# Performance work log

Hardware: AMD Instinct MI355X
Metric: run time of the kernel (lower is better)

The kernel has to match this reference:

```python
import jax, jax.numpy as jnp
import numpy as np

H = 8  # number_heads

def setup_inputs() -> dict:
    key = jax.random.key(0)
    ks = jax.random.split(key, 10)
    B, Nx, Ny, Qd, Kd, Vd = 4, 2048, 2048, 512, 512, 512
    s = 0.02
    return {
        "X": jax.random.normal(ks[0], (B, Nx, Qd), jnp.float32),
        "Y": jax.random.normal(ks[1], (B, Ny, Kd), jnp.float32),
        "Wq": jax.random.normal(ks[2], (Vd, Qd), jnp.float32) * s,
        "bq": jax.random.normal(ks[3], (Vd,), jnp.float32) * s,
        "Wk": jax.random.normal(ks[4], (Vd, Kd), jnp.float32) * s,
        "bk": jax.random.normal(ks[5], (Vd,), jnp.float32) * s,
        "Wv": jax.random.normal(ks[6], (Vd, Kd), jnp.float32) * s,
        "bv": jax.random.normal(ks[7], (Vd,), jnp.float32) * s,
        "Wo": jax.random.normal(ks[8], (Vd, Vd), jnp.float32) * s,
        "bo": jax.random.normal(ks[9], (Vd,), jnp.float32) * s,
    }

def reference(X, Y, Wq, bq, Wk, bk, Wv, bv, Wo, bo):
    B, Nq, _ = X.shape
    Nk = Y.shape[1]
    Vd = Wq.shape[0]
    d = Vd // H  # head dim (dim_split)
    # QKV projections (torch Linear: x @ W^T + b)
    Q = (X @ Wq.T + bq).reshape(B, Nq, H, d)
    K = (Y @ Wk.T + bk).reshape(B, Nk, H, d)
    V = (Y @ Wv.T + bv).reshape(B, Nk, H, d)
    # attention: softmax(Q K^T / sqrt(d)) per head
    scores = jnp.einsum("bqhd,bkhd->bhqk", Q, K) / jnp.sqrt(jnp.float32(d))
    attn = jax.nn.softmax(scores, axis=-1)
    # residual on Q (pre-output-proj), per the original: O = Q_split + Attn @ V_split
    O = Q + jnp.einsum("bhqk,bkhd->bqhd", attn, V)
    O = O.reshape(B, Nq, Vd)  # concat heads back
    return O @ Wo.T + bo
```

## Files before the change

### kernel.cpp

```cpp
#include <hip/hip_runtime.h>
#include <hip/hip_bf16.h>

typedef unsigned short u16;
typedef __attribute__((ext_vector_type(4))) float f32x4;
typedef __attribute__((ext_vector_type(16))) float f32x16;
typedef __attribute__((ext_vector_type(8))) short bf16x8;
typedef __attribute__((ext_vector_type(4))) int i32x4;
typedef __attribute__((ext_vector_type(4))) unsigned short u16x4;

#define DEVI static __device__ __forceinline__

DEVI u16 f2bf(float f) {
  __hip_bfloat16 h = __float2bfloat16(f);
  return *reinterpret_cast<u16*>(&h);
}
DEVI float bf2f(u16 u) {
  unsigned int x = ((unsigned int)u) << 16;
  return __uint_as_float(x);
}
DEVI float exp2a(float x) {
  float r;
  asm("v_exp_f32 %0, %1" : "=v"(r) : "v"(x));
  return r;
}
DEVI int cvtpk(float lo, float hi) {
  int r;
  asm("v_cvt_pk_bf16_f32 %0, %1, %2" : "=v"(r) : "v"(lo), "v"(hi));
  return r;
}
DEVI f32x16 mfma32(bf16x8 a, bf16x8 b, f32x16 c) {
  return __builtin_amdgcn_mfma_f32_32x32x16_bf16(a, b, c, 0, 0, 0);
}
DEVI float xhalf_sum(float x) {
  float a = x, b;
  asm volatile("v_mov_b32 %0, %1" : "=v"(b) : "v"(x));
  asm volatile("v_permlane32_swap_b32 %0, %1" : "+v"(a), "+v"(b));
  return a + b;
}

DEVI void gload_lds16(const void* g, void* l) {
  __builtin_amdgcn_global_load_lds(
      (const __attribute__((address_space(1))) unsigned int*)g,
      (__attribute__((address_space(3))) unsigned int*)l, 16, 0, 0);
}

#define BAR() __builtin_amdgcn_s_barrier()
#define WAITV0() asm volatile("s_waitcnt vmcnt(0)" ::: "memory")
#define WAITV4() asm volatile("s_waitcnt vmcnt(4)" ::: "memory")

__global__ __launch_bounds__(256) void k_convall(
    const float* __restrict__ X, const float* __restrict__ Y,
    const float* __restrict__ Wq, const float* __restrict__ Wk,
    const float* __restrict__ Wv, const float* __restrict__ Wo,
    u16* __restrict__ Xb, u16* __restrict__ Yb, u16* __restrict__ Wb) {
  long i = ((long)blockIdx.x * 256 + threadIdx.x) * 8;
  const float* s;
  u16* d;
  long off;
  if (i < 4194304) {
    s = X; d = Xb; off = i;
  } else if (i < 8388608) {
    s = Y; d = Yb; off = i - 4194304;
  } else {
    long w = (i - 8388608) >> 18;
    off = (i - 8388608) & 262143;
    s = w == 0 ? Wq : w == 1 ? Wk : w == 2 ? Wv : Wo;
    d = Wb + w * 262144;
  }
  f32x4 a = *(const f32x4*)(s + off);
  f32x4 b = *(const f32x4*)(s + off + 4);
  bf16x8 v;
#pragma unroll
  for (int j = 0; j < 4; ++j) {
    v[j]     = (short)f2bf(a[j]);
    v[4 + j] = (short)f2bf(b[j]);
  }
  *(bf16x8*)(d + off) = v;
}

struct GemmAcc { f32x4 acc[4][2]; };

DEVI void gemm_body(const u16* __restrict__ A, const u16* __restrict__ Bw,
                    int m0, int n0, char* sm, GemmAcc& G) {
  const int tid = threadIdx.x;
  const int wid = tid >> 6, lane = tid & 63;
  const int g = lane >> 4, li = lane & 15;
  const int wr = wid >> 1, wc = wid & 1;

  int arow[4], acol[4];
#pragma unroll
  for (int i = 0; i < 4; ++i) {
    int P0 = ((i * 4 + wid) << 10) + lane * 16;
    int L0 = P0 ^ (((P0 >> 7) & 7) << 4);
    arow[i] = L0 >> 7;
    acol[i] = L0 & 127;
  }

#pragma unroll
  for (int mr = 0; mr < 4; ++mr)
#pragma unroll
    for (int nr = 0; nr < 2; ++nr) G.acc[mr][nr] = (f32x4){0.f, 0.f, 0.f, 0.f};

  auto stage = [&](int kt, int half) {
    char* As = sm + half * 24576;
    char* Bs = As + 16384;
    const int k0b = kt * 128;
#pragma unroll
    for (int i = 0; i < 4; ++i)
      gload_lds16((const char*)A + (size_t)(m0 + arow[i]) * 1024 + k0b + acol[i],
                  As + ((i * 4 + wid) << 10));
#pragma unroll
    for (int i = 0; i < 2; ++i)
      gload_lds16((const char*)Bw + (size_t)(n0 + arow[i]) * 1024 + k0b + acol[i],
                  Bs + ((i * 4 + wid) << 10));
  };

  stage(0, 0);
#pragma unroll 1
  for (int kt = 0; kt < 8; ++kt) {
    const int half = kt & 1;
    if (kt < 7) {
      stage(kt + 1, half ^ 1);
      asm volatile("s_waitcnt vmcnt(6)" ::: "memory");
    } else {
      asm volatile("s_waitcnt vmcnt(0)" ::: "memory");
    }
    BAR();
    const char* As = sm + half * 24576;
    const char* Bs = As + 16384;
#pragma unroll
    for (int ks = 0; ks < 2; ++ks) {
      bf16x8 af[4], bfr[2];
#pragma unroll
      for (int mr = 0; mr < 4; ++mr) {
        int row = wr * 64 + mr * 16 + li;
        int L = row * 128 + ks * 64 + g * 16;
        int P = L ^ ((row & 7) << 4);
        af[mr] = *(const bf16x8*)(As + P);
      }
#pragma unroll
      for (int nr = 0; nr < 2; ++nr) {
        int row = wc * 32 + nr * 16 + li;
        int L = row * 128 + ks * 64 + g * 16;
        int P = L ^ ((row & 7) << 4);
        bfr[nr] = *(const bf16x8*)(Bs + P);
      }
#pragma unroll
      for (int mr = 0; mr < 4; ++mr)
#pragma unroll
        for (int nr = 0; nr < 2; ++nr)
          G.acc[mr][nr] = __builtin_amdgcn_mfma_f32_16x16x32_bf16(
              af[mr], bfr[nr], G.acc[mr][nr], 0, 0, 0);
    }
    BAR();
  }
}

__global__ __launch_bounds__(256) void k_gemm_qkv(
    const u16* __restrict__ Xb, const u16* __restrict__ Yb,
    const u16* __restrict__ Wall, const float* __restrict__ bq,
    const float* __restrict__ bk, const float* __restrict__ bv,
    u16* __restrict__ Qb, u16* __restrict__ Kb, u16* __restrict__ Vtb) {
  __shared__ __align__(16) char sm[49152];
  const int z = blockIdx.z;
  int lin = blockIdx.x + 8 * blockIdx.y;
  int xcd = lin & 7, slot = lin >> 3;

  const u16 *Ag, *Bg;
  int m0, n0;
  if (z == 2) {
    Ag = Wall + 2 * 262144;
    Bg = Yb;
    m0 = (slot >> 4) * 128;
    n0 = (xcd * 16 + (slot & 15)) * 64;
  } else {
    Ag = z ? Yb : Xb;
    Bg = Wall + (size_t)z * 262144;
    m0 = (xcd * 8 + (slot >> 3)) * 128;
    n0 = (slot & 7) * 64;
  }

  GemmAcc G;
  gemm_body(Ag, Bg, m0, n0, sm, G);

  const int tid = threadIdx.x;
  const int wid = tid >> 6, lane = tid & 63;
  const int g = lane >> 4, li = lane & 15;
  const int wr = wid >> 1, wc = wid & 1;

  if (z <= 1) {
    u16* Cout = z ? Kb : Qb;
    const float* bias = z ? bk : bq;
#pragma unroll
    for (int nr = 0; nr < 2; ++nr) {
      int col = n0 + wc * 32 + nr * 16 + li;
      float bvv = bias[col];
#pragma unroll
      for (int mr = 0; mr < 4; ++mr) {
#pragma unroll
        for (int j = 0; j < 4; ++j) {
          int row = m0 + wr * 64 + mr * 16 + g * 4 + j;
          float v = G.acc[mr][nr][j] + bvv;
          int b = row >> 11, nn = row & 2047, h = col >> 6, dd = col & 63;
          Cout[(((size_t)(b * 8 + h) << 11) + nn) * 64 + dd] = f2bf(v);
        }
      }
    }
  } else {
#pragma unroll
    for (int mr = 0; mr < 4; ++mr) {
#pragma unroll
      for (int j = 0; j < 4; ++j) {
        int row = m0 + wr * 64 + mr * 16 + g * 4 + j;
        float bvv = bv[row];
        int hh = row >> 6, dd = row & 63;
#pragma unroll
        for (int nr = 0; nr < 2; ++nr) {
          int col = n0 + wc * 32 + nr * 16 + li;
          int b = col >> 11, nn = col & 2047;
          Vtb[(((size_t)(b * 8 + hh) * 64) + dd) * 2048 + nn] =
              f2bf(G.acc[mr][nr][j] + bvv);
        }
      }
    }
  }
}

__global__ __launch_bounds__(256) void k_gemm_out(const u16* __restrict__ A,
                                                  const u16* __restrict__ Bw,
                                                  const float* __restrict__ bias,
                                                  float* __restrict__ Cout) {
  __shared__ __align__(16) char sm[49152];
  int lin = blockIdx.x + 8 * blockIdx.y;
  int xcd = lin & 7, slot = lin >> 3;
  int by = xcd * 8 + (slot >> 3), bx = slot & 7;
  const int m0 = by * 128, n0 = bx * 64;

  GemmAcc G;
  gemm_body(A, Bw, m0, n0, sm, G);

  const int tid = threadIdx.x;
  const int wid = tid >> 6, lane = tid & 63;
  const int g = lane >> 4, li = lane & 15;
  const int wr = wid >> 1, wc = wid & 1;
#pragma unroll
  for (int nr = 0; nr < 2; ++nr) {
    int col = n0 + wc * 32 + nr * 16 + li;
    float bvv = bias[col];
#pragma unroll
    for (int mr = 0; mr < 4; ++mr) {
#pragma unroll
      for (int j = 0; j < 4; ++j) {
        int row = m0 + wr * 64 + mr * 16 + g * 4 + j;
        Cout[(size_t)row * 512 + col] = G.acc[mr][nr][j] + bvv;
      }
    }
  }
}

DEVI void attn_tile64(const char* L, int KB, const int* v4, const bf16x8* qf,
                      f32x16& o0, f32x16& o1, float& lsum) {
  const int VB = KB + 8192;
  const f32x16 Z = {};
  f32x16 s0, s1;
  bf16x8 kf;
  kf = *(const bf16x8*)(L + KB + v4[0]);        s0 = mfma32(kf, qf[0], Z);
  kf = *(const bf16x8*)(L + KB + 4096 + v4[0]); s1 = mfma32(kf, qf[0], Z);
  kf = *(const bf16x8*)(L + KB + v4[1]);        s0 = mfma32(kf, qf[1], s0);
  kf = *(const bf16x8*)(L + KB + 4096 + v4[1]); s1 = mfma32(kf, qf[1], s1);
  kf = *(const bf16x8*)(L + KB + v4[2]);        s0 = mfma32(kf, qf[2], s0);
  kf = *(const bf16x8*)(L + KB + 4096 + v4[2]); s1 = mfma32(kf, qf[2], s1);
  kf = *(const bf16x8*)(L + KB + v4[3]);        s0 = mfma32(kf, qf[3], s0);
  kf = *(const bf16x8*)(L + KB + 4096 + v4[3]); s1 = mfma32(kf, qf[3], s1);

#pragma unroll
  for (int i = 0; i < 16; ++i) s0[i] = exp2a(s0[i]);
#pragma unroll
  for (int i = 0; i < 16; ++i) s1[i] = exp2a(s1[i]);
  float t8[8];
#pragma unroll
  for (int i = 0; i < 8; ++i)
    t8[i] = (s0[2 * i] + s0[2 * i + 1]) + (s1[2 * i] + s1[2 * i + 1]);
  lsum += ((t8[0] + t8[1]) + (t8[2] + t8[3])) + ((t8[4] + t8[5]) + (t8[6] + t8[7]));

#pragma unroll
  for (int half = 0; half < 2; ++half) {
    const f32x16& sp = half ? s1 : s0;
#pragma unroll
    for (int kt = 0; kt < 2; ++kt) {
      const int base = kt * 8;
      int a0 = cvtpk(sp[base + 0], sp[base + 1]);
      int a1 = cvtpk(sp[base + 2], sp[base + 3]);
      int b0 = cvtpk(sp[base + 4], sp[base + 5]);
      int b1 = cvtpk(sp[base + 6], sp[base + 7]);
      asm volatile("v_permlane32_swap_b32 %0, %1" : "+v"(a0), "+v"(b0));
      asm volatile("v_permlane32_swap_b32 %0, %1" : "+v"(a1), "+v"(b1));
      i32x4 pi = {a0, a1, b0, b1};
      bf16x8 pb = __builtin_bit_cast(bf16x8, pi);
      const int s = half * 2 + kt;
      bf16x8 va = *(const bf16x8*)(L + VB + v4[s]);
      o0 = mfma32(va, pb, o0);
      va = *(const bf16x8*)(L + VB + 4096 + v4[s]);
      o1 = mfma32(va, pb, o1);
    }
  }
}

__global__ __launch_bounds__(512, 4) void k_attn(const u16* __restrict__ Qb,
                                                 const u16* __restrict__ Kb,
                                                 const u16* __restrict__ Vt,
                                                 u16* __restrict__ Ob) {
  __shared__ __align__(16) char lds[65536];
  const int tid = threadIdx.x, wid = tid >> 6, lane = tid & 63;
  const int li = lane & 31, h = lane >> 5;
  const int grp = wid >> 2, w4 = wid & 3;

  const int lin = blockIdx.x;
  const int xcd = lin & 7, slot = lin >> 3;
  const int bh = xcd * 4 + (slot >> 4);
  const int qt = slot & 15;
  const int start = (slot * 3) & 15;

  const u16* Qh = Qb + ((size_t)bh << 11) * 64;
  const u16* Kh = Kb + ((size_t)bh << 11) * 64;
  const u16* Vh = Vt + (size_t)bh * 64 * 2048;

  int v4[4];
  {
    const int swz = (li & 7) << 4;
#pragma unroll
    for (int s = 0; s < 4; ++s) v4[s] = li * 128 + ((s * 32 + h * 16) ^ swz);
  }

  const int q = qt * 128 + w4 * 32 + li;
  const float C2 = 0.18033688f;
  bf16x8 qf[4];
#pragma unroll
  for (int k4 = 0; k4 < 4; ++k4) {
    bf16x8 f = *(const bf16x8*)(Qh + (size_t)q * 64 + k4 * 16 + h * 8);
    bf16x8 r;
#pragma unroll
    for (int e = 0; e < 4; ++e) {
      int p = cvtpk(bf2f((u16)f[2 * e]) * C2, bf2f((u16)f[2 * e + 1]) * C2);
      r[2 * e]     = (short)(p & 0xffff);
      r[2 * e + 1] = (short)((unsigned)p >> 16);
    }
    qf[k4] = r;
  }

  char* gb = lds + grp * 32768;
  const char* Lg = gb;
  int ksrc[2], vsrc[2];
#pragma unroll
  for (int j = 0; j < 2; ++j) {
    int P0 = w4 * 2048 + j * 1024 + lane * 16;
    int L0 = P0 ^ (((P0 >> 7) & 7) << 4);
    ksrc[j] = L0;
    vsrc[j] = (L0 >> 7) * 4096 + (L0 & 127);
  }

  auto T = [&](int n) { return grp * 16 + ((start + n) & 15); };
  auto stage = [&](int tt, int bb) {
#pragma unroll
    for (int j = 0; j < 2; ++j)
      gload_lds16((const char*)Kh + (size_t)tt * 8192 + ksrc[j],
                  gb + bb + w4 * 2048 + j * 1024);
#pragma unroll
    for (int j = 0; j < 2; ++j)
      gload_lds16((const char*)Vh + (size_t)tt * 128 + vsrc[j],
                  gb + bb + 8192 + w4 * 2048 + j * 1024);
  };

  f32x16 o0 = {}, o1 = {};
  float lsum = 0.f;

  stage(T(0), 0);
  stage(T(1), 16384);
  WAITV4();
  BAR();

#pragma unroll 1
  for (int it = 0; it < 14; ++it) {
    const int cur = (it & 1) * 16384;
    attn_tile64(Lg, cur, v4, qf, o0, o1, lsum);
    BAR();
    stage(T(it + 2), cur);
    WAITV4();
    BAR();
  }
  attn_tile64(Lg, 0, v4, qf, o0, o1, lsum);
  WAITV0();
  BAR();
  attn_tile64(Lg, 16384, v4, qf, o0, o1, lsum);

  __syncthreads();
  if (grp == 1) {
#pragma unroll
    for (int j = 0; j < 8; ++j) {
      const f32x16& o = (j < 4) ? o0 : o1;
      const int s2 = (j & 3) * 4;
      f32x4 c = {o[s2 + 0], o[s2 + 1], o[s2 + 2], o[s2 + 3]};
      *(f32x4*)(lds + w4 * 8192 + j * 1024 + lane * 16) = c;
    }
    ((float*)(lds + 32768))[w4 * 64 + lane] = lsum;
  }
  __syncthreads();
  if (grp == 0) {
#pragma unroll
    for (int j = 0; j < 8; ++j) {
      f32x4 c = *(const f32x4*)(lds + w4 * 8192 + j * 1024 + lane * 16);
      f32x16& o = (j < 4) ? o0 : o1;
      const int s2 = (j & 3) * 4;
      o[s2 + 0] += c[0]; o[s2 + 1] += c[1]; o[s2 + 2] += c[2]; o[s2 + 3] += c[3];
    }
    lsum += ((const float*)(lds + 32768))[w4 * 64 + lane];
    const float inv = 1.0f / xhalf_sum(lsum);

    const int b = bh >> 3, head = bh & 7;
    u16* orow = Ob + ((size_t)(b * 2048 + q)) * 512 + head * 64;
    const u16* qrow = Qh + (size_t)q * 64;
#pragma unroll
    for (int dt = 0; dt < 2; ++dt) {
      const f32x16& o = dt ? o1 : o0;
#pragma unroll
      for (int s2 = 0; s2 < 4; ++s2) {
        int d0 = dt * 32 + s2 * 8 + h * 4;
        u16x4 qv = *(const u16x4*)(qrow + d0);
        u16x4 w;
#pragma unroll
        for (int j = 0; j < 4; ++j)
          w[j] = f2bf(fmaf(o[s2 * 4 + j], inv, bf2f(qv[j])));
        *(u16x4*)(orow + d0) = w;
      }
    }
  }
}

extern "C" void kernel_launch(void* const* d_in, const int* in_sizes, int n_in,
                              void* d_out, int out_size, void* d_ws, size_t ws_size,
                              hipStream_t stream) {
  const float* X  = (const float*)d_in[0];
  const float* Y  = (const float*)d_in[1];
  const float* Wq = (const float*)d_in[2];
  const float* bq = (const float*)d_in[3];
  const float* Wk = (const float*)d_in[4];
  const float* bk = (const float*)d_in[5];
  const float* Wv = (const float*)d_in[6];
  const float* bv = (const float*)d_in[7];
  const float* Wo = (const float*)d_in[8];
  const float* bo = (const float*)d_in[9];

  char* ws = (char*)d_ws;
  u16* Xb  = (u16*)(ws);
  u16* Yb  = (u16*)(ws + (size_t)(8  << 20));
  u16* Wb  = (u16*)(ws + (size_t)(16 << 20));
  u16* Qb  = (u16*)(ws + (size_t)(18 << 20));
  u16* Kb  = (u16*)(ws + (size_t)(26 << 20));
  u16* Vtb = (u16*)(ws + (size_t)(34 << 20));
  u16* Ob  = (u16*)(ws + (size_t)(42 << 20));

  k_convall<<<4608, 256, 0, stream>>>(X, Y, Wq, Wk, Wv, Wo, Xb, Yb, Wb);

  k_gemm_qkv<<<dim3(8, 64, 3), 256, 0, stream>>>(Xb, Yb, Wb, bq, bk, bv, Qb, Kb, Vtb);

  k_attn<<<512, 512, 0, stream>>>(Qb, Kb, Vtb, Ob);

  k_gemm_out<<<dim3(8, 64), 256, 0, stream>>>(Ob, Wb + 3 * 262144, bo, (float*)d_out);
}
```

Baseline: 86.80 us.

## Process two query tiles per wave in attention to reuse K/V fragments

```diff
diff --git a/kernel.cpp b/kernel.cpp
--- a/kernel.cpp
+++ b/kernel.cpp
@@ -258,67 +258,85 @@
   }
 }
 
-DEVI void attn_tile64(const char* L, int KB, const int* v4, const bf16x8* qf,
-                      f32x16& o0, f32x16& o1, float& lsum) {
-  const int VB = KB + 8192;
+DEVI void attn_phase(const char* L, int kb, int vb, const int* v4, int sv0, int sv1,
+                     const bf16x8* qfA, const bf16x8* qfB,
+                     f32x16& oA0, f32x16& oA1, f32x16& oB0, f32x16& oB1,
+                     float& lsumA, float& lsumB) {
   const f32x16 Z = {};
-  f32x16 s0, s1;
+  f32x16 sA, sB;
   bf16x8 kf;
-  kf = *(const bf16x8*)(L + KB + v4[0]);        s0 = mfma32(kf, qf[0], Z);
-  kf = *(const bf16x8*)(L + KB + 4096 + v4[0]); s1 = mfma32(kf, qf[0], Z);
-  kf = *(const bf16x8*)(L + KB + v4[1]);        s0 = mfma32(kf, qf[1], s0);
-  kf = *(const bf16x8*)(L + KB + 4096 + v4[1]); s1 = mfma32(kf, qf[1], s1);
-  kf = *(const bf16x8*)(L + KB + v4[2]);        s0 = mfma32(kf, qf[2], s0);
-  kf = *(const bf16x8*)(L + KB + 4096 + v4[2]); s1 = mfma32(kf, qf[2], s1);
-  kf = *(const bf16x8*)(L + KB + v4[3]);        s0 = mfma32(kf, qf[3], s0);
-  kf = *(const bf16x8*)(L + KB + 4096 + v4[3]); s1 = mfma32(kf, qf[3], s1);
-
-#pragma unroll
-  for (int i = 0; i < 16; ++i) s0[i] = exp2a(s0[i]);
-#pragma unroll
-  for (int i = 0; i < 16; ++i) s1[i] = exp2a(s1[i]);
-  float t8[8];
-#pragma unroll
-  for (int i = 0; i < 8; ++i)
-    t8[i] = (s0[2 * i] + s0[2 * i + 1]) + (s1[2 * i] + s1[2 * i + 1]);
-  lsum += ((t8[0] + t8[1]) + (t8[2] + t8[3])) + ((t8[4] + t8[5]) + (t8[6] + t8[7]));
-
-#pragma unroll
-  for (int half = 0; half < 2; ++half) {
-    const f32x16& sp = half ? s1 : s0;
-#pragma unroll
-    for (int kt = 0; kt < 2; ++kt) {
-      const int base = kt * 8;
-      int a0 = cvtpk(sp[base + 0], sp[base + 1]);
-      int a1 = cvtpk(sp[base + 2], sp[base + 3]);
-      int b0 = cvtpk(sp[base + 4], sp[base + 5]);
-      int b1 = cvtpk(sp[base + 6], sp[base + 7]);
-      asm volatile("v_permlane32_swap_b32 %0, %1" : "+v"(a0), "+v"(b0));
-      asm volatile("v_permlane32_swap_b32 %0, %1" : "+v"(a1), "+v"(b1));
-      i32x4 pi = {a0, a1, b0, b1};
-      bf16x8 pb = __builtin_bit_cast(bf16x8, pi);
-      const int s = half * 2 + kt;
-      bf16x8 va = *(const bf16x8*)(L + VB + v4[s]);
-      o0 = mfma32(va, pb, o0);
-      va = *(const bf16x8*)(L + VB + 4096 + v4[s]);
-      o1 = mfma32(va, pb, o1);
-    }
-  }
-}
-
-__global__ __launch_bounds__(512, 4) void k_attn(const u16* __restrict__ Qb,
+  kf = *(const bf16x8*)(L + kb + v4[0]);
+  sA = mfma32(kf, qfA[0], Z);  sB = mfma32(kf, qfB[0], Z);
+  kf = *(const bf16x8*)(L + kb + v4[1]);
+  sA = mfma32(kf, qfA[1], sA); sB = mfma32(kf, qfB[1], sB);
+  kf = *(const bf16x8*)(L + kb + v4[2]);
+  sA = mfma32(kf, qfA[2], sA); sB = mfma32(kf, qfB[2], sB);
+  kf = *(const bf16x8*)(L + kb + v4[3]);
+  sA = mfma32(kf, qfA[3], sA); sB = mfma32(kf, qfB[3], sB);
+
+  bf16x8 va0l = *(const bf16x8*)(L + vb + v4[sv0]);
+  bf16x8 va0h = *(const bf16x8*)(L + vb + 4096 + v4[sv0]);
+  bf16x8 va1l = *(const bf16x8*)(L + vb + v4[sv1]);
+  bf16x8 va1h = *(const bf16x8*)(L + vb + 4096 + v4[sv1]);
+
+#pragma unroll
+  for (int i = 0; i < 16; ++i) sA[i] = exp2a(sA[i]);
+#pragma unroll
+  for (int i = 0; i < 16; ++i) sB[i] = exp2a(sB[i]);
+  float tA[4], tB[4];
+#pragma unroll
+  for (int i = 0; i < 4; ++i) {
+    tA[i] = (sA[4 * i] + sA[4 * i + 1]) + (sA[4 * i + 2] + sA[4 * i + 3]);
+    tB[i] = (sB[4 * i] + sB[4 * i + 1]) + (sB[4 * i + 2] + sB[4 * i + 3]);
+  }
+  lsumA += (tA[0] + tA[1]) + (tA[2] + tA[3]);
+  lsumB += (tB[0] + tB[1]) + (tB[2] + tB[3]);
+
+  bf16x8 pbA[2], pbB[2];
+#pragma unroll
+  for (int kt = 0; kt < 2; ++kt) {
+    const int base = kt * 8;
+    int a0 = cvtpk(sA[base + 0], sA[base + 1]);
+    int a1 = cvtpk(sA[base + 2], sA[base + 3]);
+    int b0 = cvtpk(sA[base + 4], sA[base + 5]);
+    int b1 = cvtpk(sA[base + 6], sA[base + 7]);
+    asm volatile("v_permlane32_swap_b32 %0, %1" : "+v"(a0), "+v"(b0));
+    asm volatile("v_permlane32_swap_b32 %0, %1" : "+v"(a1), "+v"(b1));
+    i32x4 pi = {a0, a1, b0, b1};
+    pbA[kt] = __builtin_bit_cast(bf16x8, pi);
+    int c0 = cvtpk(sB[base + 0], sB[base + 1]);
+    int c1 = cvtpk(sB[base + 2], sB[base + 3]);
+    int d0 = cvtpk(sB[base + 4], sB[base + 5]);
+    int d1 = cvtpk(sB[base + 6], sB[base + 7]);
+    asm volatile("v_permlane32_swap_b32 %0, %1" : "+v"(c0), "+v"(d0));
+    asm volatile("v_permlane32_swap_b32 %0, %1" : "+v"(c1), "+v"(d1));
+    i32x4 qi = {c0, c1, d0, d1};
+    pbB[kt] = __builtin_bit_cast(bf16x8, qi);
+  }
+
+  oA0 = mfma32(va0l, pbA[0], oA0);
+  oB0 = mfma32(va0l, pbB[0], oB0);
+  oA1 = mfma32(va0h, pbA[0], oA1);
+  oB1 = mfma32(va0h, pbB[0], oB1);
+  oA0 = mfma32(va1l, pbA[1], oA0);
+  oB0 = mfma32(va1l, pbB[1], oB0);
+  oA1 = mfma32(va1h, pbA[1], oA1);
+  oB1 = mfma32(va1h, pbB[1], oB1);
+}
+
+__global__ __launch_bounds__(512, 2) void k_attn(const u16* __restrict__ Qb,
                                                  const u16* __restrict__ Kb,
                                                  const u16* __restrict__ Vt,
                                                  u16* __restrict__ Ob) {
-  __shared__ __align__(16) char lds[65536];
+  __shared__ __align__(16) char lds[67584];
   const int tid = threadIdx.x, wid = tid >> 6, lane = tid & 63;
   const int li = lane & 31, h = lane >> 5;
   const int grp = wid >> 2, w4 = wid & 3;
 
   const int lin = blockIdx.x;
   const int xcd = lin & 7, slot = lin >> 3;
-  const int bh = xcd * 4 + (slot >> 4);
-  const int qt = slot & 15;
+  const int bh = xcd * 4 + (slot >> 3);
+  const int qt = slot & 7;
   const int start = (slot * 3) & 15;
 
   const u16* Qh = Qb + ((size_t)bh << 11) * 64;
@@ -332,20 +350,26 @@
     for (int s = 0; s < 4; ++s) v4[s] = li * 128 + ((s * 32 + h * 16) ^ swz);
   }
 
-  const int q = qt * 128 + w4 * 32 + li;
+  const int qA = qt * 256 + w4 * 64 + li;
+  const int qB = qA + 32;
   const float C2 = 0.18033688f;
-  bf16x8 qf[4];
+  bf16x8 qfA[4], qfB[4];
 #pragma unroll
   for (int k4 = 0; k4 < 4; ++k4) {
-    bf16x8 f = *(const bf16x8*)(Qh + (size_t)q * 64 + k4 * 16 + h * 8);
-    bf16x8 r;
+    bf16x8 fA = *(const bf16x8*)(Qh + (size_t)qA * 64 + k4 * 16 + h * 8);
+    bf16x8 fB = *(const bf16x8*)(Qh + (size_t)qB * 64 + k4 * 16 + h * 8);
+    bf16x8 rA, rB;
 #pragma unroll
     for (int e = 0; e < 4; ++e) {
-      int p = cvtpk(bf2f((u16)f[2 * e]) * C2, bf2f((u16)f[2 * e + 1]) * C2);
-      r[2 * e]     = (short)(p & 0xffff);
-      r[2 * e + 1] = (short)((unsigned)p >> 16);
-    }
-    qf[k4] = r;
+      int pA = cvtpk(bf2f((u16)fA[2 * e]) * C2, bf2f((u16)fA[2 * e + 1]) * C2);
+      rA[2 * e]     = (short)(pA & 0xffff);
+      rA[2 * e + 1] = (short)((unsigned)pA >> 16);
+      int pB = cvtpk(bf2f((u16)fB[2 * e]) * C2, bf2f((u16)fB[2 * e + 1]) * C2);
+      rB[2 * e]     = (short)(pB & 0xffff);
+      rB[2 * e + 1] = (short)((unsigned)pB >> 16);
+    }
+    qfA[k4] = rA;
+    qfB[k4] = rB;
   }
 
   char* gb = lds + grp * 32768;
@@ -371,8 +395,8 @@
                   gb + bb + 8192 + w4 * 2048 + j * 1024);
   };
 
-  f32x16 o0 = {}, o1 = {};
-  float lsum = 0.f;
+  f32x16 oA0 = {}, oA1 = {}, oB0 = {}, oB1 = {};
+  float lsumA = 0.f, lsumB = 0.f;
 
   stage(T(0), 0);
   stage(T(1), 16384);
@@ -382,55 +406,68 @@
 #pragma unroll 1
   for (int it = 0; it < 14; ++it) {
     const int cur = (it & 1) * 16384;
-    attn_tile64(Lg, cur, v4, qf, o0, o1, lsum);
+    attn_phase(Lg, cur, cur + 8192, v4, 0, 1, qfA, qfB, oA0, oA1, oB0, oB1,
+               lsumA, lsumB);
+    attn_phase(Lg, cur + 4096, cur + 8192, v4, 2, 3, qfA, qfB, oA0, oA1, oB0, oB1,
+               lsumA, lsumB);
     BAR();
     stage(T(it + 2), cur);
     WAITV4();
     BAR();
   }
-  attn_tile64(Lg, 0, v4, qf, o0, o1, lsum);
+  attn_phase(Lg, 0, 8192, v4, 0, 1, qfA, qfB, oA0, oA1, oB0, oB1, lsumA, lsumB);
+  attn_phase(Lg, 4096, 8192, v4, 2, 3, qfA, qfB, oA0, oA1, oB0, oB1, lsumA, lsumB);
   WAITV0();
   BAR();
-  attn_tile64(Lg, 16384, v4, qf, o0, o1, lsum);
+  attn_phase(Lg, 16384, 24576, v4, 0, 1, qfA, qfB, oA0, oA1, oB0, oB1, lsumA, lsumB);
+  attn_phase(Lg, 20480, 24576, v4, 2, 3, qfA, qfB, oA0, oA1, oB0, oB1, lsumA, lsumB);
 
   __syncthreads();
   if (grp == 1) {
 #pragma unroll
-    for (int j = 0; j < 8; ++j) {
-      const f32x16& o = (j < 4) ? o0 : o1;
+    for (int j = 0; j < 16; ++j) {
+      const f32x16& o = (j < 4) ? oA0 : (j < 8) ? oA1 : (j < 12) ? oB0 : oB1;
       const int s2 = (j & 3) * 4;
       f32x4 c = {o[s2 + 0], o[s2 + 1], o[s2 + 2], o[s2 + 3]};
-      *(f32x4*)(lds + w4 * 8192 + j * 1024 + lane * 16) = c;
-    }
-    ((float*)(lds + 32768))[w4 * 64 + lane] = lsum;
+      *(f32x4*)(lds + w4 * 16384 + j * 1024 + lane * 16) = c;
+    }
+    ((float*)(lds + 65536))[w4 * 128 + lane] = lsumA;
+    ((float*)(lds + 65536))[w4 * 128 + 64 + lane] = lsumB;
   }
   __syncthreads();
   if (grp == 0) {
 #pragma unroll
-    for (int j = 0; j < 8; ++j) {
-      f32x4 c = *(const f32x4*)(lds + w4 * 8192 + j * 1024 + lane * 16);
-      f32x16& o = (j < 4) ? o0 : o1;
+    for (int j = 0; j < 16; ++j) {
+      f32x4 c = *(const f32x4*)(lds + w4 * 16384 + j * 1024 + lane * 16);
+      f32x16& o = (j < 4) ? oA0 : (j < 8) ? oA1 : (j < 12) ? oB0 : oB1;
       const int s2 = (j & 3) * 4;
       o[s2 + 0] += c[0]; o[s2 + 1] += c[1]; o[s2 + 2] += c[2]; o[s2 + 3] += c[3];
     }
-    lsum += ((const float*)(lds + 32768))[w4 * 64 + lane];
-    const float inv = 1.0f / xhalf_sum(lsum);
+    lsumA += ((const float*)(lds + 65536))[w4 * 128 + lane];
+    lsumB += ((const float*)(lds + 65536))[w4 * 128 + 64 + lane];
+    const float invA = 1.0f / xhalf_sum(lsumA);
+    const float invB = 1.0f / xhalf_sum(lsumB);
 
     const int b = bh >> 3, head = bh & 7;
-    u16* orow = Ob + ((size_t)(b * 2048 + q)) * 512 + head * 64;
-    const u16* qrow = Qh + (size_t)q * 64;
-#pragma unroll
-    for (int dt = 0; dt < 2; ++dt) {
-      const f32x16& o = dt ? o1 : o0;
-#pragma unroll
-      for (int s2 = 0; s2 < 4; ++s2) {
-        int d0 = dt * 32 + s2 * 8 + h * 4;
-        u16x4 qv = *(const u16x4*)(qrow + d0);
-        u16x4 w;
-#pragma unroll
-        for (int j = 0; j < 4; ++j)
-          w[j] = f2bf(fmaf(o[s2 * 4 + j], inv, bf2f(qv[j])));
-        *(u16x4*)(orow + d0) = w;
+#pragma unroll
+    for (int half = 0; half < 2; ++half) {
+      const int q = half ? qB : qA;
+      const float inv = half ? invB : invA;
+      u16* orow = Ob + ((size_t)(b * 2048 + q)) * 512 + head * 64;
+      const u16* qrow = Qh + (size_t)q * 64;
+#pragma unroll
+      for (int dt = 0; dt < 2; ++dt) {
+        const f32x16& o = half ? (dt ? oB1 : oB0) : (dt ? oA1 : oA0);
+#pragma unroll
+        for (int s2 = 0; s2 < 4; ++s2) {
+          int d0 = dt * 32 + s2 * 8 + h * 4;
+          u16x4 qv = *(const u16x4*)(qrow + d0);
+          u16x4 w;
+#pragma unroll
+          for (int j = 0; j < 4; ++j)
+            w[j] = f2bf(fmaf(o[s2 * 4 + j], inv, bf2f(qv[j])));
+          *(u16x4*)(orow + d0) = w;
+        }
       }
     }
   }
@@ -463,7 +500,7 @@
 
   k_gemm_qkv<<<dim3(8, 64, 3), 256, 0, stream>>>(Xb, Yb, Wb, bq, bk, bv, Qb, Kb, Vtb);
 
-  k_attn<<<512, 512, 0, stream>>>(Qb, Kb, Vtb, Ob);
+  k_attn<<<256, 512, 0, stream>>>(Qb, Kb, Vtb, Ob);
 
   k_gemm_out<<<dim3(8, 64), 256, 0, stream>>>(Ob, Wb + 3 * 262144, bo, (float*)d_out);
 }
```

Result: no change. 85.20 us (-1.8%).
